# Kernel optimization log

Hardware: AMD Instinct MI355X
Metric: run time of the kernel (lower is better)

Reference implementation:

```python
import jax, jax.numpy as jnp
import numpy as np

B, N, DIM, H, D = 1, 1024, 512, 8, 64
BC, BS, K, W = 16, 16, 8, 256   # compress blk, selection blk, top-k blocks, sliding window
C = N // BC                     # number of compression / selection blocks
SCALE = D ** -0.5
EPS = 1e-6
NEG = -1e30


def rmsnorm(x):
    return x * jax.lax.rsqrt(jnp.mean(x * x, axis=-1, keepdims=True) + EPS)


def rope(x):  # x: [B,H,N,D], GPT-NeoX style half rotation
    half = D // 2
    inv = 1.0 / (10000.0 ** (jnp.arange(half, dtype=jnp.float32) / half))
    ang = jnp.arange(x.shape[2], dtype=jnp.float32)[:, None] * inv
    cos, sin = jnp.cos(ang), jnp.sin(ang)
    x1, x2 = x[..., :half], x[..., half:]
    return jnp.concatenate([x1 * cos - x2 * sin, x2 * cos + x1 * sin], axis=-1).astype(x.dtype)


def setup_inputs():
    key = jax.random.key(0)
    ks = jax.random.split(key, 24)
    w = lambda k, shape, fan: jax.random.normal(k, shape, jnp.float32) * (fan ** -0.5)
    return {
        'x':  jax.random.normal(ks[0], (B, N, DIM), jnp.float32),
        've': jax.random.normal(ks[1], (B, N, DIM), jnp.float32),
        'x0': jax.random.normal(ks[2], (B, N, DIM), jnp.float32),
        'lambdas': jnp.array([1.0, 0.0], jnp.float32),
        'Wq': w(ks[3], (DIM, H * D), DIM),
        'Wk': w(ks[4], (DIM, H * D), DIM),
        'Wv': w(ks[5], (DIM, H * D), DIM),
        'Wo': w(ks[6], (H * D, DIM), H * D),
        'Wg': w(ks[7], (DIM, 3 * H), DIM),
        'k_pos': w(ks[8], (H, BC, D), D),
        'v_pos': w(ks[9], (H, BC, D), D),
        'Wck': w(ks[10], (BC * D, D), BC * D),
        'bck': jnp.zeros((D,), jnp.float32),
        'Wcv': w(ks[11], (BC * D, D), BC * D),
        'bcv': jnp.zeros((D,), jnp.float32),
        'k_mem': w(ks[12], (H, 1, D), D),
        'v_mem': w(ks[13], (H, 1, D), D),
        'W1': w(ks[14], (DIM, 4 * DIM), DIM),
        'W2': w(ks[15], (4 * DIM, DIM), 4 * DIM),
    }


def _nsa_attn(xn, Wq, Wk, Wv, Wo, Wg, k_pos, v_pos, Wck, bck, Wcv, bcv, k_mem, v_mem):
    q = (xn @ Wq).reshape(B, N, H, D).transpose(0, 2, 1, 3)   # [B,H,N,D]
    k = (xn @ Wk).reshape(B, N, H, D).transpose(0, 2, 1, 3)
    v = (xn @ Wv).reshape(B, N, H, D).transpose(0, 2, 1, 3)
    q, k = rope(q), rope(k)
    i_idx = jnp.arange(N)

    # ---- compressed branch: pool kv into blocks via learned linear + intra-block pos emb ----
    kb = k.reshape(B, H, C, BC, D) + k_pos[None, :, None]
    vb = v.reshape(B, H, C, BC, D) + v_pos[None, :, None]
    ck = kb.reshape(B, H, C, BC * D) @ Wck + bck              # [B,H,C,D]
    cv = vb.reshape(B, H, C, BC * D) @ Wcv + bcv
    ckf = jnp.concatenate([jnp.broadcast_to(k_mem[None], (B, H, 1, D)), ck], axis=2)
    cvf = jnp.concatenate([jnp.broadcast_to(v_mem[None], (B, H, 1, D)), cv], axis=2)
    csim = jnp.einsum('bhid,bhjd->bhij', q, ckf) * SCALE      # [B,H,N,C+1]
    past = ((jnp.arange(C) + 1) * BC - 1)[None, :] < i_idx[:, None]   # block fully in the past
    cmask = jnp.concatenate([jnp.ones((N, 1), bool), past], axis=1)   # mem kv always visible
    cattn = jax.nn.softmax(jnp.where(cmask[None, None], csim, NEG), axis=-1)
    c_out = jnp.einsum('bhij,bhjd->bhid', cattn, cvf)

    # ---- fine selection branch: top-K blocks by compressed attention importance ----
    imp = jnp.where(past[None, None], cattn[..., 1:], NEG)    # [B,H,N,C]
    vals, sel = jax.lax.top_k(imp, K)                         # [B,H,N,K]
    valid = vals >= 0.0                                       # drop picks among masked blocks
    kb_f = k.reshape(B, H, C, BS, D)
    vb_f = v.reshape(B, H, C, BS, D)
    k_sel = jnp.take_along_axis(kb_f[:, :, None], sel[..., None, None], axis=3)  # [B,H,N,K,BS,D]
    v_sel = jnp.take_along_axis(vb_f[:, :, None], sel[..., None, None], axis=3)
    own = i_idx // BS                                         # query's own block, causal inside
    k_fine = jnp.concatenate([k_sel, kb_f[:, :, own][:, :, :, None]], axis=3)    # [B,H,N,K+1,BS,D]
    v_fine = jnp.concatenate([v_sel, vb_f[:, :, own][:, :, :, None]], axis=3)
    offs = jnp.arange(BS)
    m_sel = (sel[..., None] * BS + offs <= i_idx[None, None, :, None, None]) & valid[..., None]
    m_own = jnp.broadcast_to((own[:, None] * BS + offs <= i_idx[:, None])[None, None, :, None], (B, H, N, 1, BS))
    m_fine = jnp.concatenate([m_sel, m_own], axis=3)
    fsim = jnp.where(m_fine, jnp.einsum('bhnd,bhnksd->bhnks', q, k_fine) * SCALE, NEG)
    fattn = jax.nn.softmax(fsim.reshape(B, H, N, (K + 1) * BS), axis=-1).reshape(B, H, N, K + 1, BS)
    f_out = jnp.einsum('bhnks,bhnksd->bhnd', fattn, v_fine)

    # ---- sliding window branch ----
    smask = (i_idx[None, :] <= i_idx[:, None]) & (i_idx[:, None] - i_idx[None, :] < W)
    ssim = jnp.where(smask[None, None], jnp.einsum('bhid,bhjd->bhij', q, k) * SCALE, NEG)
    s_out = jnp.einsum('bhij,bhjd->bhid', jax.nn.softmax(ssim, axis=-1), v)

    # ---- per-head sigmoid gates combine the three strategies ----
    gates = jax.nn.sigmoid(xn @ Wg).reshape(B, N, H, 3).transpose(0, 2, 1, 3)  # [B,H,N,3]
    o = gates[..., 0:1] * c_out + gates[..., 1:2] * f_out + gates[..., 2:3] * s_out
    return o.transpose(0, 2, 1, 3).reshape(B, N, H * D) @ Wo


def reference(x, ve, x0, lambdas, Wq, Wk, Wv, Wo, Wg, k_pos, v_pos, Wck, bck, Wcv, bcv, k_mem, v_mem, W1, W2):
    # ve is accepted by NSABlock.forward but never consumed in this block
    x = lambdas[0] * x + lambdas[1] * x0
    x = x + _nsa_attn(rmsnorm(x), Wq, Wk, Wv, Wo, Wg, k_pos, v_pos, Wck, bck, Wcv, bcv, k_mem, v_mem)
    x = x + jnp.square(jax.nn.relu(rmsnorm(x) @ W1)) @ W2
    return x
```

## Files before the change

kernel.cpp:

```cpp
#include <hip/hip_runtime.h>
#include <math.h>

#define NTOK 1024
#define DIMM 512
#define NH 8
#define HD 64
#define BCB 16
#define BSB 16
#define KSEL 8
#define WWIN 256
#define CBLK 64
#define SCALE 0.125f
#define EPSV 1e-6f
#define NEGV -1e30f

typedef short bf16x8 __attribute__((ext_vector_type(8)));
typedef float f32x4 __attribute__((ext_vector_type(4)));

__device__ inline ushort f2b(float f) {
  union { float f; unsigned int u; } c; c.f = f;
  unsigned int u = c.u;
  return (ushort)((u + 0x7FFFu + ((u >> 16) & 1u)) >> 16);
}
__device__ inline float b2f(ushort h) {
  union { unsigned int u; float f; } c; c.u = ((unsigned int)h) << 16;
  return c.f;
}

__device__ inline float wred_max(float v) {
#pragma unroll
  for (int off = 1; off < 64; off <<= 1) v = fmaxf(v, __shfl_xor(v, off));
  return v;
}
__device__ inline float wred_sum(float v) {
#pragma unroll
  for (int off = 1; off < 64; off <<= 1) v += __shfl_xor(v, off);
  return v;
}

__global__ void __launch_bounds__(256)
k_resid_rms(const float* __restrict__ x, const float* __restrict__ x0,
            const float* __restrict__ lam, float* __restrict__ xr,
            float* __restrict__ xn) {
  int row = blockIdx.x, tid = threadIdx.x;
  float l0 = lam[0], l1 = lam[1];
  size_t b = (size_t)row * DIMM;
  float a0 = l0 * x[b + tid]       + l1 * x0[b + tid];
  float a1 = l0 * x[b + tid + 256] + l1 * x0[b + tid + 256];
  xr[b + tid] = a0; xr[b + tid + 256] = a1;
  float ss = a0 * a0 + a1 * a1;
  __shared__ float sm[8];
  for (int o = 32; o > 0; o >>= 1) ss += __shfl_down(ss, o);
  int lane = tid & 63, wid = tid >> 6;
  if (lane == 0) sm[wid] = ss;
  __syncthreads();
  if (tid == 0) {
    float s = sm[0] + sm[1] + sm[2] + sm[3];
    sm[0] = rsqrtf(s / (float)DIMM + EPSV);
  }
  __syncthreads();
  float r = sm[0];
  xn[b + tid] = a0 * r; xn[b + tid + 256] = a1 * r;
}

__global__ void __launch_bounds__(256)
k_rms_bf(const float* __restrict__ xin, ushort* __restrict__ y) {
  int row = blockIdx.x, tid = threadIdx.x;
  size_t b = (size_t)row * DIMM;
  float a0 = xin[b + tid], a1 = xin[b + tid + 256];
  float ss = a0 * a0 + a1 * a1;
  __shared__ float sm[8];
  for (int o = 32; o > 0; o >>= 1) ss += __shfl_down(ss, o);
  int lane = tid & 63, wid = tid >> 6;
  if (lane == 0) sm[wid] = ss;
  __syncthreads();
  if (tid == 0) {
    float s = sm[0] + sm[1] + sm[2] + sm[3];
    sm[0] = rsqrtf(s / (float)DIMM + EPSV);
  }
  __syncthreads();
  float r = sm[0];
  y[b + tid] = f2b(a0 * r); y[b + tid + 256] = f2b(a1 * r);
}

struct WtrDesc { const float* src; ushort* dh; ushort* dl; int K; int Nsrc; int Npad; };
struct WtrPack { WtrDesc d[9]; int cum[9]; };

__global__ void __launch_bounds__(256)
k_wtr_all(WtrPack pk) {
  int gb = blockIdx.x;
  int e = 0;
  while (gb >= pk.cum[e]) e++;
  int start = e ? pk.cum[e - 1] : 0;
  WtrDesc dd = pk.d[e];
  int local = gb - start;
  int XT = dd.Npad >> 5;
  int bx = local % XT, by = local / XT;
  __shared__ float t[32][33];
  int n0 = bx * 32, k0 = by * 32;
  int tx = threadIdx.x, ty = threadIdx.y;
#pragma unroll
  for (int i = 0; i < 32; i += 8)
    t[ty + i][tx] = (n0 + tx < dd.Nsrc)
        ? dd.src[(size_t)(k0 + ty + i) * dd.Nsrc + n0 + tx] : 0.f;
  __syncthreads();
#pragma unroll
  for (int i = 0; i < 32; i += 8) {
    float vv = t[tx][ty + i];
    ushort h = f2b(vv);
    size_t di = (size_t)(n0 + ty + i) * dd.K + k0 + tx;
    dd.dh[di] = h;
    if (dd.dl) dd.dl[di] = f2b(vv - b2f(h));
  }
}

__global__ void __launch_bounds__(256)
k_gemm_w1(const ushort* __restrict__ A, const ushort* __restrict__ BT,
          ushort* __restrict__ Co) {
  const int Kd = 512, Nd = 2048;
  __shared__ ushort As[128 * 40];
  __shared__ ushort Bs[64 * 40];
  int tid = threadIdx.x;
  int lane = tid & 63, w = tid >> 6;
  int rb = blockIdx.y * 128, cb = blockIdx.x * 64;
  int wm = (w >> 1) * 64, wn = (w & 1) * 32;
  int quad = lane >> 4, l15 = lane & 15;
  int srA = tid >> 1, scA = (tid & 1) * 16;
  int srB = tid >> 2, scB = (tid & 3) * 8;

  f32x4 acc[4][2];
#pragma unroll
  for (int i = 0; i < 4; i++)
#pragma unroll
    for (int j = 0; j < 2; j++) acc[i][j] = (f32x4){0.f, 0.f, 0.f, 0.f};

  const ushort* ap = A  + (size_t)(rb + srA) * Kd + scA;
  const ushort* bp = BT + (size_t)(cb + srB) * Kd + scB;
  ushort* aw = &As[srA * 40 + scA];
  ushort* bw = &Bs[srB * 40 + scB];

  int4 pa0 = *(const int4*)ap;
  int4 pa1 = *(const int4*)(ap + 8);
  int4 pb  = *(const int4*)bp;

  for (int k0 = 0; k0 < Kd; k0 += 32) {
    if (k0) __syncthreads();
    *(int4*)aw = pa0; *(int4*)(aw + 8) = pa1;
    *(int4*)bw = pb;
    __syncthreads();
    if (k0 + 32 < Kd) {
      pa0 = *(const int4*)(ap + k0 + 32);
      pa1 = *(const int4*)(ap + k0 + 40);
      pb  = *(const int4*)(bp + k0 + 32);
    }
    bf16x8 af[4], bfr[2];
#pragma unroll
    for (int t = 0; t < 4; t++)
      af[t] = *(const bf16x8*)&As[(wm + t * 16 + l15) * 40 + quad * 8];
#pragma unroll
    for (int t = 0; t < 2; t++)
      bfr[t] = *(const bf16x8*)&Bs[(wn + t * 16 + l15) * 40 + quad * 8];
#pragma unroll
    for (int i = 0; i < 4; i++)
#pragma unroll
      for (int j = 0; j < 2; j++)
        acc[i][j] = __builtin_amdgcn_mfma_f32_16x16x32_bf16(af[i], bfr[j],
                                                            acc[i][j], 0, 0, 0);
  }

#pragma unroll
  for (int i = 0; i < 4; i++) {
#pragma unroll
    for (int j = 0; j < 2; j++) {
      int col = cb + wn + j * 16 + l15;
#pragma unroll
      for (int r = 0; r < 4; r++) {
        int row = rb + wm + i * 16 + quad * 4 + r;
        float t = fmaxf(acc[i][j][r], 0.f);
        Co[(size_t)row * Nd + col] = f2b(t * t);
      }
    }
  }
}

__global__ void __launch_bounds__(256)
k_gemm_w2(const ushort* __restrict__ A, const ushort* __restrict__ BT,
          float* __restrict__ P0, float* __restrict__ P1) {
  const int Kd = 2048;
  __shared__ ushort As[64 * 40];
  __shared__ ushort Bs[64 * 40];
  int tid = threadIdx.x;
  int lane = tid & 63, w = tid >> 6;
  int rb = blockIdx.y * 64, cb = blockIdx.x * 64;
  int kb = blockIdx.z * 1024;
  int wm = (w >> 1) * 32, wn = (w & 1) * 32;
  int quad = lane >> 4, l15 = lane & 15;
  int srow = tid >> 2, scol = (tid & 3) * 8;

  f32x4 acc[2][2];
#pragma unroll
  for (int i = 0; i < 2; i++)
#pragma unroll
    for (int j = 0; j < 2; j++) acc[i][j] = (f32x4){0.f, 0.f, 0.f, 0.f};

  const ushort* ap = A  + (size_t)(rb + srow) * Kd + kb + scol;
  const ushort* bp = BT + (size_t)(cb + srow) * Kd + kb + scol;
  ushort* aw = &As[srow * 40 + scol];
  ushort* bw = &Bs[srow * 40 + scol];

  int4 pa = *(const int4*)ap;
  int4 pb = *(const int4*)bp;

  for (int k0 = 0; k0 < 1024; k0 += 32) {
    if (k0) __syncthreads();
    *(int4*)aw = pa;
    *(int4*)bw = pb;
    __syncthreads();
    if (k0 + 32 < 1024) {
      pa = *(const int4*)(ap + k0 + 32);
      pb = *(const int4*)(bp + k0 + 32);
    }
    bf16x8 af[2], bfr[2];
#pragma unroll
    for (int t = 0; t < 2; t++) {
      af[t]  = *(const bf16x8*)&As[(wm + t * 16 + l15) * 40 + quad * 8];
      bfr[t] = *(const bf16x8*)&Bs[(wn + t * 16 + l15) * 40 + quad * 8];
    }
#pragma unroll
    for (int i = 0; i < 2; i++)
#pragma unroll
      for (int j = 0; j < 2; j++)
        acc[i][j] = __builtin_amdgcn_mfma_f32_16x16x32_bf16(af[i], bfr[j],
                                                            acc[i][j], 0, 0, 0);
  }

  float* pbuf = blockIdx.z ? P1 : P0;
#pragma unroll
  for (int i = 0; i < 2; i++) {
#pragma unroll
    for (int j = 0; j < 2; j++) {
      int col = cb + wn + j * 16 + l15;
#pragma unroll
      for (int r = 0; r < 4; r++) {
        int row = rb + wm + i * 16 + quad * 4 + r;
        pbuf[(size_t)row * 512 + col] = acc[i][j][r];
      }
    }
  }
}

__global__ void __launch_bounds__(256)
k_w2fin(const float* __restrict__ x2, const float* __restrict__ p0,
        const float* __restrict__ p1, float* __restrict__ out) {
  int idx = blockIdx.x * 256 + threadIdx.x;
  out[idx] = x2[idx] + p0[idx] + p1[idx];
}

__global__ void __launch_bounds__(256)
k_gemm_wo(const float* __restrict__ cg, const float* __restrict__ fg,
          const float* __restrict__ sg, const float* __restrict__ gates,
          const ushort* __restrict__ BT, const float* __restrict__ Res,
          float* __restrict__ Co) {
  __shared__ ushort As[64 * 40];
  __shared__ ushort Bs[64 * 40];
  int tid = threadIdx.x;
  int lane = tid & 63, wave = tid >> 6;
  int rb = blockIdx.y * 64, cb = blockIdx.x * 64;
  int wm = (wave >> 1) * 32, wn = (wave & 1) * 32;
  int q = lane >> 4, l15 = lane & 15;
  int srow = tid >> 2, scol = (tid & 3) * 8;

  f32x4 acc[2][2];
#pragma unroll
  for (int i = 0; i < 2; i++)
#pragma unroll
    for (int j = 0; j < 2; j++) acc[i][j] = (f32x4){0.f, 0.f, 0.f, 0.f};

  int row = rb + srow;
  const ushort* bp = BT + (size_t)(cb + srow) * 512 + scol;
  ushort* aw = &As[srow * 40 + scol];
  ushort* bw = &Bs[srow * 40 + scol];

  for (int k0 = 0; k0 < 512; k0 += 32) {
    int colb = k0 + scol;
    int hh = colb >> 6;
    const float* gp = gates + (size_t)row * 24 + hh * 3;
    float g0 = gp[0], g1 = gp[1], g2 = gp[2];
    size_t off = (size_t)row * 512 + colb;
    float4 c0 = *(const float4*)(cg + off), c1 = *(const float4*)(cg + off + 4);
    float4 f0 = *(const float4*)(fg + off), f1 = *(const float4*)(fg + off + 4);
    float4 s0 = *(const float4*)(sg + off), s1 = *(const float4*)(sg + off + 4);
    float va[8] = {g0 * c0.x + g1 * f0.x + g2 * s0.x,
                   g0 * c0.y + g1 * f0.y + g2 * s0.y,
                   g0 * c0.z + g1 * f0.z + g2 * s0.z,
                   g0 * c0.w + g1 * f0.w + g2 * s0.w,
                   g0 * c1.x + g1 * f1.x + g2 * s1.x,
                   g0 * c1.y + g1 * f1.y + g2 * s1.y,
                   g0 * c1.z + g1 * f1.z + g2 * s1.z,
                   g0 * c1.w + g1 * f1.w + g2 * s1.w};
    ushort h[8];
#pragma unroll
    for (int e = 0; e < 8; e++) h[e] = f2b(va[e]);
    *(int4*)aw = *(int4*)h;
    *(int4*)bw = *(const int4*)(bp + k0);
    __syncthreads();
    bf16x8 af[2], bfr[2];
#pragma unroll
    for (int t = 0; t < 2; t++) {
      af[t]  = *(const bf16x8*)&As[(wm + t * 16 + l15) * 40 + q * 8];
      bfr[t] = *(const bf16x8*)&Bs[(wn + t * 16 + l15) * 40 + q * 8];
    }
#pragma unroll
    for (int i = 0; i < 2; i++)
#pragma unroll
      for (int j = 0; j < 2; j++)
        acc[i][j] = __builtin_amdgcn_mfma_f32_16x16x32_bf16(af[i], bfr[j],
                                                            acc[i][j], 0, 0, 0);
    __syncthreads();
  }

#pragma unroll
  for (int i = 0; i < 2; i++) {
#pragma unroll
    for (int j = 0; j < 2; j++) {
      int col = cb + wn + j * 16 + l15;
#pragma unroll
      for (int r = 0; r < 4; r++) {
        int rr = rb + wm + i * 16 + q * 4 + r;
        Co[(size_t)rr * 512 + col] = acc[i][j][r] + Res[(size_t)rr * 512 + col];
      }
    }
  }
}

__global__ void __launch_bounds__(256)
k_gemm_qkv(const float* __restrict__ A, const ushort* __restrict__ BTh,
           const ushort* __restrict__ BTl, float* __restrict__ Co,
           float* __restrict__ vhm, float* __restrict__ gates, int Kd) {
  __shared__ ushort Ash[64 * 40];
  __shared__ ushort Asl[64 * 40];
  __shared__ ushort Bsh[64 * 40];
  __shared__ ushort Bsl[64 * 40];
  int tid = threadIdx.x;
  int lane = tid & 63, wave = tid >> 6;
  int rb = blockIdx.y * 64, cb = blockIdx.x * 64;
  int wm = (wave >> 1) * 32, wn = (wave & 1) * 32;
  int q = lane >> 4, l15 = lane & 15;
  int srow = tid >> 2, scol = (tid & 3) * 8;

  f32x4 acc[2][2];
#pragma unroll
  for (int i = 0; i < 2; i++)
#pragma unroll
    for (int j = 0; j < 2; j++) acc[i][j] = (f32x4){0.f, 0.f, 0.f, 0.f};

  const float*  ap  = A   + (size_t)(rb + srow) * Kd + scol;
  const ushort* bph = BTh + (size_t)(cb + srow) * Kd + scol;
  const ushort* bpl = BTl + (size_t)(cb + srow) * Kd + scol;
  ushort* awh = &Ash[srow * 40 + scol];
  ushort* awl = &Asl[srow * 40 + scol];
  ushort* bwh = &Bsh[srow * 40 + scol];
  ushort* bwl = &Bsl[srow * 40 + scol];

  for (int k0 = 0; k0 < Kd; k0 += 32) {
    float4 a0 = *(const float4*)(ap + k0);
    float4 a1 = *(const float4*)(ap + k0 + 4);
    float va[8] = {a0.x, a0.y, a0.z, a0.w, a1.x, a1.y, a1.z, a1.w};
    ushort hh[8], hl[8];
#pragma unroll
    for (int e = 0; e < 8; e++) {
      hh[e] = f2b(va[e]);
      hl[e] = f2b(va[e] - b2f(hh[e]));
    }
    *(int4*)awh = *(int4*)hh;
    *(int4*)awl = *(int4*)hl;
    *(int4*)bwh = *(const int4*)(bph + k0);
    *(int4*)bwl = *(const int4*)(bpl + k0);
    __syncthreads();
    bf16x8 afh[2], afl[2], bfh[2], bfl[2];
#pragma unroll
    for (int t = 0; t < 2; t++) {
      int ar = (wm + t * 16 + l15) * 40 + q * 8;
      int br = (wn + t * 16 + l15) * 40 + q * 8;
      afh[t] = *(const bf16x8*)&Ash[ar];
      afl[t] = *(const bf16x8*)&Asl[ar];
      bfh[t] = *(const bf16x8*)&Bsh[br];
      bfl[t] = *(const bf16x8*)&Bsl[br];
    }
#pragma unroll
    for (int i = 0; i < 2; i++)
#pragma unroll
      for (int j = 0; j < 2; j++) {
        acc[i][j] = __builtin_amdgcn_mfma_f32_16x16x32_bf16(afh[i], bfh[j],
                                                            acc[i][j], 0, 0, 0);
        acc[i][j] = __builtin_amdgcn_mfma_f32_16x16x32_bf16(afh[i], bfl[j],
                                                            acc[i][j], 0, 0, 0);
        acc[i][j] = __builtin_amdgcn_mfma_f32_16x16x32_bf16(afl[i], bfh[j],
                                                            acc[i][j], 0, 0, 0);
      }
    __syncthreads();
  }

  const size_t NW = (size_t)NTOK * DIMM;
#pragma unroll
  for (int i = 0; i < 2; i++) {
#pragma unroll
    for (int j = 0; j < 2; j++) {
      int col = cb + wn + j * 16 + l15;
#pragma unroll
      for (int r = 0; r < 4; r++) {
        int row = rb + wm + i * 16 + q * 4 + r;
        float vv = acc[i][j][r];
        if (cb >= 1536) {
          int c24 = col - 1536;
          if (c24 < 24)
            gates[(size_t)row * 24 + c24] = 1.f / (1.f + expf(-vv));
        } else if (col >= 1024) {
          int c = col - 1024;
          vhm[(size_t)(c >> 6) * 65536 + (size_t)row * 64 + (c & 63)] = vv;
        } else {
          Co[(size_t)(col >> 9) * NW + (size_t)row * 512 + (col & 511)] = vv;
        }
      }
    }
  }
}

__global__ void __launch_bounds__(256)
k_rope(float* __restrict__ q, const float* __restrict__ k,
       float* __restrict__ khm, ushort* __restrict__ khm_bf,
       const float* __restrict__ vhm, ushort* __restrict__ vhm_bf) {
  int idx = blockIdx.x * 256 + threadIdx.x;
  int seg = idx >> 18;
  if (seg >= 2) {
    int ci = idx - 524288;
    if (ci < 131072) {
      float4 t = *(const float4*)(vhm + (size_t)ci * 4);
      ushort4 u = {f2b(t.x), f2b(t.y), f2b(t.z), f2b(t.w)};
      *(ushort4*)(vhm_bf + (size_t)ci * 4) = u;
    }
    return;
  }
  int r = idx & 262143;
  int j = r & 31;
  int h = (r >> 5) & 7;
  int n = r >> 8;
  float inv = powf(10000.f, -(float)j / 32.f);
  float ang = (float)n * inv;
  float sn, cs;
  sincosf(ang, &sn, &cs);
  size_t base = (size_t)n * DIMM + h * HD + j;
  if (seg == 0) {
    float x1 = q[base], x2 = q[base + 32];
    q[base] = x1 * cs - x2 * sn;
    q[base + 32] = x2 * cs + x1 * sn;
  } else {
    float x1 = k[base], x2 = k[base + 32];
    float o1 = x1 * cs - x2 * sn;
    float o2 = x2 * cs + x1 * sn;
    size_t ob = (size_t)h * 65536 + (size_t)n * 64 + j;
    khm[ob] = o1;
    khm[ob + 32] = o2;
    khm_bf[ob] = f2b(o1);
    khm_bf[ob + 32] = f2b(o2);
  }
}

__global__ void __launch_bounds__(256)
k_ckcv_m(const float* __restrict__ khm, const float* __restrict__ vhm,
         const float* __restrict__ k_pos, const float* __restrict__ v_pos,
         const ushort* __restrict__ WckTh, const ushort* __restrict__ WckTl,
         const ushort* __restrict__ WcvTh, const ushort* __restrict__ WcvTl,
         const float* __restrict__ bck, const float* __restrict__ bcv,
         float* __restrict__ ckb, float* __restrict__ cvb) {
  int h = blockIdx.x, kv = blockIdx.y;
  const float* src = kv ? vhm : khm;
  const float* pos = kv ? v_pos : k_pos;
  const ushort* WTh = kv ? WcvTh : WckTh;
  const ushort* WTl = kv ? WcvTl : WckTl;
  const float* bias = kv ? bcv : bck;
  float* outp = kv ? cvb : ckb;

  __shared__ ushort Ash[64 * 72], Asl[64 * 72];
  __shared__ ushort Bsh[64 * 72], Bsl[64 * 72];
  int tid = threadIdx.x;
  int lane = tid & 63, wave = tid >> 6;
  int wm = (wave >> 1) * 32, wn = (wave & 1) * 32;
  int q = lane >> 4, l15 = lane & 15;
  int srow = tid >> 2;
  int e0 = (tid & 3) * 16;

  f32x4 acc[2][2];
#pragma unroll
  for (int i = 0; i < 2; i++)
#pragma unroll
    for (int j = 0; j < 2; j++) acc[i][j] = (f32x4){0.f, 0.f, 0.f, 0.f};

  for (int t = 0; t < 16; t++) {
    const float* ar = src + (size_t)h * 65536 + (size_t)(srow * 16 + t) * 64 + e0;
    const float* pr = pos + (size_t)(h * 16 + t) * HD + e0;
    ushort hh[16], hl[16];
#pragma unroll
    for (int u = 0; u < 4; u++) {
      float4 av = *(const float4*)(ar + u * 4);
      float4 pv = *(const float4*)(pr + u * 4);
      float vals[4] = {av.x + pv.x, av.y + pv.y, av.z + pv.z, av.w + pv.w};
#pragma unroll
      for (int e = 0; e < 4; e++) {
        ushort hb = f2b(vals[e]);
        hh[u * 4 + e] = hb;
        hl[u * 4 + e] = f2b(vals[e] - b2f(hb));
      }
    }
    *(int4*)&Ash[srow * 72 + e0]     = *(int4*)&hh[0];
    *(int4*)&Ash[srow * 72 + e0 + 8] = *(int4*)&hh[8];
    *(int4*)&Asl[srow * 72 + e0]     = *(int4*)&hl[0];
    *(int4*)&Asl[srow * 72 + e0 + 8] = *(int4*)&hl[8];
    const ushort* bh = WTh + (size_t)srow * 1024 + t * 64 + e0;
    const ushort* bl = WTl + (size_t)srow * 1024 + t * 64 + e0;
    *(int4*)&Bsh[srow * 72 + e0]     = *(const int4*)bh;
    *(int4*)&Bsh[srow * 72 + e0 + 8] = *(const int4*)(bh + 8);
    *(int4*)&Bsl[srow * 72 + e0]     = *(const int4*)bl;
    *(int4*)&Bsl[srow * 72 + e0 + 8] = *(const int4*)(bl + 8);
    __syncthreads();
#pragma unroll
    for (int sub = 0; sub < 2; sub++) {
      bf16x8 afh[2], afl[2], bfh[2], bfl[2];
#pragma unroll
      for (int ti = 0; ti < 2; ti++) {
        int ar2 = (wm + ti * 16 + l15) * 72 + sub * 32 + q * 8;
        int br2 = (wn + ti * 16 + l15) * 72 + sub * 32 + q * 8;
        afh[ti] = *(const bf16x8*)&Ash[ar2];
        afl[ti] = *(const bf16x8*)&Asl[ar2];
        bfh[ti] = *(const bf16x8*)&Bsh[br2];
        bfl[ti] = *(const bf16x8*)&Bsl[br2];
      }
#pragma unroll
      for (int i = 0; i < 2; i++)
#pragma unroll
        for (int j = 0; j < 2; j++) {
          acc[i][j] = __builtin_amdgcn_mfma_f32_16x16x32_bf16(afh[i], bfh[j],
                                                              acc[i][j], 0, 0, 0);
          acc[i][j] = __builtin_amdgcn_mfma_f32_16x16x32_bf16(afh[i], bfl[j],
                                                              acc[i][j], 0, 0, 0);
          acc[i][j] = __builtin_amdgcn_mfma_f32_16x16x32_bf16(afl[i], bfh[j],
                                                              acc[i][j], 0, 0, 0);
        }
    }
    __syncthreads();
  }

#pragma unroll
  for (int i = 0; i < 2; i++) {
#pragma unroll
    for (int j = 0; j < 2; j++) {
      int d = wn + j * 16 + l15;
      float bv = bias[d];
#pragma unroll
      for (int r = 0; r < 4; r++) {
        int c = wm + i * 16 + q * 4 + r;
        outp[((size_t)h * 64 + c) * 64 + d] = acc[i][j][r] + bv;
      }
    }
  }
}

__global__ void __launch_bounds__(256)
k_cmp(const float* __restrict__ qg, const float* __restrict__ ckb,
      const float* __restrict__ cvb, const float* __restrict__ k_mem,
      const float* __restrict__ v_mem, float* __restrict__ cout,
      int* __restrict__ sel) {
  int h = blockIdx.y, i0 = blockIdx.x * 16;
  int tid = threadIdx.x, lane = tid & 63, w = tid >> 6;
  __shared__ float ckt[64][65];
  __shared__ float cvs[64][65];
  __shared__ float qs[16][64];
  __shared__ float kms[64], vms[64];
  __shared__ float sp[4][64];

#pragma unroll
  for (int r = 0; r < 4; r++) {
    int f = r * 256 + tid;
    int c = f >> 4, d0 = (f & 15) * 4;
    float4 t = *(const float4*)(ckb + ((size_t)h * 64 + c) * 64 + d0);
    ckt[d0][c] = t.x; ckt[d0 + 1][c] = t.y; ckt[d0 + 2][c] = t.z; ckt[d0 + 3][c] = t.w;
    float4 u = *(const float4*)(cvb + ((size_t)h * 64 + c) * 64 + d0);
    cvs[c][d0] = u.x; cvs[c][d0 + 1] = u.y; cvs[c][d0 + 2] = u.z; cvs[c][d0 + 3] = u.w;
  }
  {
    int r = tid >> 4, d0 = (tid & 15) * 4;
    float4 t = *(const float4*)(qg + (size_t)(i0 + r) * DIMM + h * HD + d0);
    qs[r][d0] = t.x; qs[r][d0 + 1] = t.y; qs[r][d0 + 2] = t.z; qs[r][d0 + 3] = t.w;
  }
  if (tid < 64) kms[tid] = k_mem[h * HD + tid];
  else if (tid < 128) vms[tid - 64] = v_mem[h * HD + tid - 64];
  __syncthreads();

  for (int s = 0; s < 4; s++) {
    int ql = w * 4 + s, qi = i0 + ql;
    float dot = 0.f, dm = 0.f;
#pragma unroll 8
    for (int e = 0; e < 64; e++) {
      float qe = qs[ql][e];
      dot = fmaf(qe, ckt[e][lane], dot);
      dm  = fmaf(qe, kms[e], dm);
    }
    bool vis = (lane * BCB + BCB - 1) < qi;
    float sj = vis ? dot * SCALE : NEGV;
    float smem = dm * SCALE;
    float m = wred_max(fmaxf(sj, smem));
    float p = expf(sj - m);
    float pmem = expf(smem - m);
    float l = wred_sum(p) + pmem;
    float inv = 1.f / l;

    float impv = vis ? p : NEGV;
#pragma unroll
    for (int kk = 0; kk < KSEL; kk++) {
      float bv = impv; int bi = lane;
#pragma unroll
      for (int off = 32; off > 0; off >>= 1) {
        float ov = __shfl_xor(bv, off);
        int   oi = __shfl_xor(bi, off);
        if (ov > bv || (ov == bv && oi < bi)) { bv = ov; bi = oi; }
      }
      if (lane == 0) sel[((size_t)h * NTOK + qi) * KSEL + kk] = (bv >= 0.f) ? bi : -1;
      if (lane == bi) impv = NEGV;
    }

    sp[w][lane] = p;
    float od = pmem * vms[lane];
#pragma unroll 8
    for (int j = 0; j < 64; j++) od = fmaf(sp[w][j], cvs[j][lane], od);
    cout[(size_t)qi * DIMM + h * HD + lane] = od * inv;
  }
}

__global__ void __launch_bounds__(256)
k_swin(const float* __restrict__ qg, const ushort* __restrict__ khm_bf,
       const ushort* __restrict__ vhm_bf, float* __restrict__ sout) {
  int h = blockIdx.y, i0 = blockIdx.x * 64;
  int tid = threadIdx.x, lane = tid & 63, w = tid >> 6;
  int quad = lane >> 4, l15 = lane & 15;

  __shared__ ushort Kt[64 * 72];
  __shared__ ushort VT[64 * 72];
  __shared__ ushort Qs[64 * 72];
  __shared__ ushort Ps[4][16 * 72];

#pragma unroll
  for (int it = 0; it < 4; it++) {
    int f = it * 256 + tid;
    int r = f >> 4, d0 = (f & 15) * 4;
    float4 t = *(const float4*)(qg + (size_t)(i0 + r) * DIMM + h * HD + d0);
    ushort4 u = {f2b(t.x), f2b(t.y), f2b(t.z), f2b(t.w)};
    *(ushort4*)&Qs[r * 72 + d0] = u;
  }

  int lo = i0 - (WWIN - 1); if (lo < 0) lo = 0;
  int jb_lo = lo >> 6, jb_hi = (i0 + 63) >> 6;

  float mrow[4], lrow[4];
  f32x4 Of[4];
#pragma unroll
  for (int r = 0; r < 4; r++) { mrow[r] = NEGV; lrow[r] = 0.f; }
#pragma unroll
  for (int d = 0; d < 4; d++) Of[d] = (f32x4){0.f, 0.f, 0.f, 0.f};

  for (int jb = jb_lo; jb <= jb_hi; jb++) {
    __syncthreads();
#pragma unroll
    for (int it = 0; it < 2; it++) {
      int f = it * 256 + tid;
      int r = f >> 3, c8 = (f & 7) * 8;
      const ushort* kp = khm_bf + (size_t)h * 65536 + (size_t)(jb * 64 + r) * 64 + c8;
      *(int4*)&Kt[r * 72 + c8] = *(const int4*)kp;
      const ushort* vp = vhm_bf + (size_t)h * 65536 + (size_t)(jb * 64 + r) * 64 + c8;
      ushort vv[8];
      *(int4*)vv = *(const int4*)vp;
#pragma unroll
      for (int e = 0; e < 8; e++) VT[(c8 + e) * 72 + r] = vv[e];
    }
    __syncthreads();

    bf16x8 qa[2];
#pragma unroll
    for (int c = 0; c < 2; c++)
      qa[c] = *(const bf16x8*)&Qs[(w * 16 + l15) * 72 + c * 32 + quad * 8];

    f32x4 sc[4];
#pragma unroll
    for (int ks = 0; ks < 4; ks++) {
      f32x4 a = (f32x4){0.f, 0.f, 0.f, 0.f};
#pragma unroll
      for (int c = 0; c < 2; c++) {
        bf16x8 kb = *(const bf16x8*)&Kt[(ks * 16 + l15) * 72 + c * 32 + quad * 8];
        a = __builtin_amdgcn_mfma_f32_16x16x32_bf16(qa[c], kb, a, 0, 0, 0);
      }
      sc[ks] = a;
    }

    float pm[4][4], rmax[4];
#pragma unroll
    for (int r = 0; r < 4; r++) rmax[r] = NEGV;
#pragma unroll
    for (int ks = 0; ks < 4; ks++) {
      int gj = jb * 64 + ks * 16 + l15;
#pragma unroll
      for (int r = 0; r < 4; r++) {
        int qi = i0 + w * 16 + quad * 4 + r;
        bool vis = (gj <= qi) && (qi - gj < WWIN);
        float s = vis ? sc[ks][r] * SCALE : NEGV;
        pm[ks][r] = s;
        rmax[r] = fmaxf(rmax[r], s);
      }
    }
#pragma unroll
    for (int off = 1; off < 16; off <<= 1)
#pragma unroll
      for (int r = 0; r < 4; r++)
        rmax[r] = fmaxf(rmax[r], __shfl_xor(rmax[r], off));

    float alpha[4], rsum[4];
#pragma unroll
    for (int r = 0; r < 4; r++) {
      float newm = fmaxf(mrow[r], rmax[r]);
      alpha[r] = expf(mrow[r] - newm);
      mrow[r] = newm;
      rsum[r] = 0.f;
    }
#pragma unroll
    for (int ks = 0; ks < 4; ks++)
#pragma unroll
      for (int r = 0; r < 4; r++) {
        float p = expf(pm[ks][r] - mrow[r]);
        pm[ks][r] = p;
        rsum[r] += p;
      }
#pragma unroll
    for (int off = 1; off < 16; off <<= 1)
#pragma unroll
      for (int r = 0; r < 4; r++)
        rsum[r] += __shfl_xor(rsum[r], off);
#pragma unroll
    for (int r = 0; r < 4; r++)
      lrow[r] = lrow[r] * alpha[r] + rsum[r];

#pragma unroll
    for (int ks = 0; ks < 4; ks++)
#pragma unroll
      for (int r = 0; r < 4; r++)
        Ps[w][(quad * 4 + r) * 72 + ks * 16 + l15] = f2b(pm[ks][r]);
#pragma unroll
    for (int d = 0; d < 4; d++)
#pragma unroll
      for (int r = 0; r < 4; r++)
        Of[d][r] *= alpha[r];

#pragma unroll
    for (int c = 0; c < 2; c++) {
      bf16x8 pa = *(const bf16x8*)&Ps[w][l15 * 72 + c * 32 + quad * 8];
#pragma unroll
      for (int d = 0; d < 4; d++) {
        bf16x8 vb = *(const bf16x8*)&VT[(d * 16 + l15) * 72 + c * 32 + quad * 8];
        Of[d] = __builtin_amdgcn_mfma_f32_16x16x32_bf16(pa, vb, Of[d], 0, 0, 0);
      }
    }
  }

#pragma unroll
  for (int d = 0; d < 4; d++)
#pragma unroll
    for (int r = 0; r < 4; r++) {
      int qi = i0 + w * 16 + quad * 4 + r;
      sout[(size_t)qi * DIMM + h * HD + d * 16 + l15] = Of[d][r] / lrow[r];
    }
}

__global__ void __launch_bounds__(256)
k_fine(const float* __restrict__ qg, const ushort* __restrict__ khm_bf,
       const ushort* __restrict__ vhm_bf, const int* __restrict__ sel,
       float* __restrict__ fout) {
  int i = blockIdx.x, h = blockIdx.y;
  int tid = threadIdx.x, lane = tid & 63, w = tid >> 6;
  __shared__ float qsh[64];
  __shared__ ushort vsb[144 * 64];
  __shared__ float sp[144];
  __shared__ int selS[8];
  __shared__ float mred[4], sredS[4];
  __shared__ float pacc[4][64];

  int own = i >> 4;
  if (tid < 64) qsh[tid] = qg[(size_t)i * DIMM + h * HD + tid];
  if (tid >= 64 && tid < 72)
    selS[tid - 64] = sel[((size_t)h * NTOK + i) * KSEL + tid - 64];
  __syncthreads();

  const ushort* kbase = khm_bf + (size_t)h * 65536;
  const ushort* vbase = vhm_bf + (size_t)h * 65536;

#pragma unroll
  for (int it = 0; it < 5; it++) {
    int idx = it * 256 + tid;
    if (idx < 1152) {
      int row = idx >> 3, c8 = (idx & 7) * 8;
      int kk = row >> 4;
      int bidx = (kk < KSEL) ? selS[kk] : own;
      if (bidx < 0) bidx = 0;
      *(int4*)&vsb[row * 64 + c8] =
          *(const int4*)(vbase + (size_t)(bidx * BSB + (row & 15)) * 64 + c8);
    }
  }

  float s_loc = NEGV;
  bool active = (tid < 144);
  if (active) {
    int kk = tid >> 4;
    int bidx; bool vis;
    if (kk < KSEL) {
      bidx = selS[kk];
      vis = (bidx >= 0);
      if (!vis) bidx = 0;
    } else {
      bidx = own;
      vis = (tid - 128) <= (i & 15);
    }
    const ushort* kr = kbase + (size_t)(bidx * BSB + (tid & 15)) * 64;
    float dot = 0.f;
#pragma unroll
    for (int e8 = 0; e8 < 8; e8++) {
      ushort kv[8];
      *(int4*)kv = *(const int4*)(kr + e8 * 8);
#pragma unroll
      for (int e = 0; e < 8; e++)
        dot = fmaf(qsh[e8 * 8 + e], b2f(kv[e]), dot);
    }
    s_loc = vis ? dot * SCALE : NEGV;
  }
  float mw = wred_max(s_loc);
  if (lane == 0) mred[w] = mw;
  __syncthreads();
  float m = fmaxf(fmaxf(mred[0], mred[1]), fmaxf(mred[2], mred[3]));
  float p = active ? expf(s_loc - m) : 0.f;
  float sw = wred_sum(p);
  if (lane == 0) sredS[w] = sw;
  if (active) sp[tid] = p;
  __syncthreads();
  float l = sredS[0] + sredS[1] + sredS[2] + sredS[3];

  float acc = 0.f;
  int j0 = w * 36;
#pragma unroll 6
  for (int jj = 0; jj < 36; jj++) {
    int j = j0 + jj;
    acc = fmaf(sp[j], b2f(vsb[j * 64 + lane]), acc);
  }
  pacc[w][lane] = acc;
  __syncthreads();
  if (w == 0)
    fout[(size_t)i * DIMM + h * HD + lane] =
        (pacc[0][lane] + pacc[1][lane] + pacc[2][lane] + pacc[3][lane]) / l;
}

extern "C" void kernel_launch(void* const* d_in, const int* in_sizes, int n_in,
                              void* d_out, int out_size, void* d_ws, size_t ws_size,
                              hipStream_t stream) {
  const float* x     = (const float*)d_in[0];
  const float* ve    = (const float*)d_in[1]; (void)ve;
  const float* x0    = (const float*)d_in[2];
  const float* lam   = (const float*)d_in[3];
  const float* Wq    = (const float*)d_in[4];
  const float* Wk    = (const float*)d_in[5];
  const float* Wv    = (const float*)d_in[6];
  const float* Wo    = (const float*)d_in[7];
  const float* Wg    = (const float*)d_in[8];
  const float* k_pos = (const float*)d_in[9];
  const float* v_pos = (const float*)d_in[10];
  const float* Wck   = (const float*)d_in[11];
  const float* bck   = (const float*)d_in[12];
  const float* Wcv   = (const float*)d_in[13];
  const float* bcv   = (const float*)d_in[14];
  const float* k_mem = (const float*)d_in[15];
  const float* v_mem = (const float*)d_in[16];
  const float* W1    = (const float*)d_in[17];
  const float* W2    = (const float*)d_in[18];
  float* out = (float*)d_out;
  float* ws  = (float*)d_ws;

  const size_t NW = (size_t)NTOK * DIMM;
  float* xr    = ws;
  float* xn    = ws + 1 * NW;
  float* q     = ws + 2 * NW;
  float* k     = ws + 3 * NW;
  float* vhm   = ws + 4 * NW;
  float* coutb = ws + 5 * NW;
  float* foutb = ws + 6 * NW;
  float* soutb = ws + 7 * NW;
  float* x2    = ws + 8 * NW;
  float* khm   = x2;
  float* gates = ws + 9 * NW;
  float* ckb   = gates + 32768;
  float* cvb   = ckb + 32768;
  int*   selb  = (int*)(cvb + 32768);
  ushort* qkvTh = (ushort*)(cvb + 32768 + 65536);
  ushort* qkvTl = qkvTh + 1600 * 512;
  ushort* WoT   = qkvTl + 1600 * 512;
  ushort* W1T   = WoT   + 512 * 512;
  ushort* W2T   = W1T   + 2048 * 512;
  ushort* WckTh = W2T   + 512 * 2048;
  ushort* WckTl = WckTh + 64 * 1024;
  ushort* WcvTh = WckTl + 64 * 1024;
  ushort* WcvTl = WcvTh + 64 * 1024;
  ushort* ybf = (ushort*)xr;
  ushort* h1b = (ushort*)q;
  float* p0 = xn;
  float* p1 = vhm;
  ushort* khm_bf = (ushort*)xn;
  ushort* vhm_bf = khm_bf + 524288;

  WtrPack pk;
  pk.d[0] = {Wq, qkvTh,              qkvTl,              512, 512,  512};
  pk.d[1] = {Wk, qkvTh + 512 * 512,  qkvTl + 512 * 512,  512, 512,  512};
  pk.d[2] = {Wv, qkvTh + 1024 * 512, qkvTl + 1024 * 512, 512, 512,  512};
  pk.d[3] = {Wo, WoT, nullptr,  512, 512,  512};
  pk.d[4] = {W1, W1T, nullptr,  512, 2048, 2048};
  pk.d[5] = {W2, W2T, nullptr, 2048, 512,  512};
  pk.d[6] = {Wck, WckTh, WckTl, 1024, 64, 64};
  pk.d[7] = {Wcv, WcvTh, WcvTl, 1024, 64, 64};
  pk.d[8] = {Wg, qkvTh + 1536 * 512, qkvTl + 1536 * 512, 512, 24, 64};
  int cum = 0;
  for (int e = 0; e < 9; e++) {
    cum += (pk.d[e].Npad / 32) * (pk.d[e].K / 32);
    pk.cum[e] = cum;
  }
  k_wtr_all<<<cum, dim3(32, 8), 0, stream>>>(pk);

  k_resid_rms<<<NTOK, 256, 0, stream>>>(x, x0, lam, xr, xn);

  k_gemm_qkv<<<dim3(25, NTOK / 64), 256, 0, stream>>>(
      xn, qkvTh, qkvTl, q, vhm, gates, 512);
  k_rope<<<2560, 256, 0, stream>>>(q, k, khm, khm_bf, vhm, vhm_bf);

  k_ckcv_m<<<dim3(NH, 2), 256, 0, stream>>>(khm, vhm, k_pos, v_pos,
                                            WckTh, WckTl, WcvTh, WcvTl,
                                            bck, bcv, ckb, cvb);
  k_cmp<<<dim3(NTOK / 16, NH), 256, 0, stream>>>(q, ckb, cvb, k_mem, v_mem,
                                                 coutb, selb);
  k_swin<<<dim3(NTOK / 64, NH), 256, 0, stream>>>(q, khm_bf, vhm_bf, soutb);
  k_fine<<<dim3(NTOK, NH), 256, 0, stream>>>(q, khm_bf, vhm_bf, selb, foutb);

  k_gemm_wo<<<dim3(512 / 64, NTOK / 64), 256, 0, stream>>>(
      coutb, foutb, soutb, gates, WoT, xr, x2);

  k_rms_bf<<<NTOK, 256, 0, stream>>>(x2, ybf);
  k_gemm_w1<<<dim3(2048 / 64, NTOK / 128), 256, 0, stream>>>(ybf, W1T, h1b);
  k_gemm_w2<<<dim3(512 / 64, NTOK / 64, 2), 256, 0, stream>>>(h1b, W2T, p0, p1);
  k_w2fin<<<NW / 256, 256, 0, stream>>>(x2, p0, p1, out);
}
```

Before: 279.7 us.

## Split-K Wo GEMM, split ckcv and swin grids, drop split-bf16 for V/gates

The Wo projection is split over K into two partial buffers, and the residual add is fused into the following RMSNorm kernel. The compression-weight GEMM is split into two M-halves and the sliding-window kernel uses 32-row tiles with 128 threads, both to raise block counts on small grids. The QKV GEMM skips the hi/lo correction MFMAs for column blocks at or above 1024 (V and gates), which cuts compute but lowers precision for V.

Result: faster. 270.1 us (-3.4%).

```diff
diff --git a/kernel.cpp b/kernel.cpp
--- a/kernel.cpp
+++ b/kernel.cpp
@@ -64,10 +64,14 @@
 }
 
 __global__ void __launch_bounds__(256)
-k_rms_bf(const float* __restrict__ xin, ushort* __restrict__ y) {
+k_rms_bf(const float* __restrict__ xr, const float* __restrict__ p0,
+         const float* __restrict__ p1, float* __restrict__ x2,
+         ushort* __restrict__ y) {
   int row = blockIdx.x, tid = threadIdx.x;
   size_t b = (size_t)row * DIMM;
-  float a0 = xin[b + tid], a1 = xin[b + tid + 256];
+  float a0 = xr[b + tid]       + p0[b + tid]       + p1[b + tid];
+  float a1 = xr[b + tid + 256] + p0[b + tid + 256] + p1[b + tid + 256];
+  x2[b + tid] = a0; x2[b + tid + 256] = a1;
   float ss = a0 * a0 + a1 * a1;
   __shared__ float sm[8];
   for (int o = 32; o > 0; o >>= 1) ss += __shfl_down(ss, o);
@@ -259,13 +263,14 @@
 __global__ void __launch_bounds__(256)
 k_gemm_wo(const float* __restrict__ cg, const float* __restrict__ fg,
           const float* __restrict__ sg, const float* __restrict__ gates,
-          const ushort* __restrict__ BT, const float* __restrict__ Res,
-          float* __restrict__ Co) {
+          const ushort* __restrict__ BT, float* __restrict__ P0,
+          float* __restrict__ P1) {
   __shared__ ushort As[64 * 40];
   __shared__ ushort Bs[64 * 40];
   int tid = threadIdx.x;
   int lane = tid & 63, wave = tid >> 6;
   int rb = blockIdx.y * 64, cb = blockIdx.x * 64;
+  int kb = blockIdx.z * 256;
   int wm = (wave >> 1) * 32, wn = (wave & 1) * 32;
   int q = lane >> 4, l15 = lane & 15;
   int srow = tid >> 2, scol = (tid & 3) * 8;
@@ -277,12 +282,12 @@
     for (int j = 0; j < 2; j++) acc[i][j] = (f32x4){0.f, 0.f, 0.f, 0.f};
 
   int row = rb + srow;
-  const ushort* bp = BT + (size_t)(cb + srow) * 512 + scol;
+  const ushort* bp = BT + (size_t)(cb + srow) * 512 + kb + scol;
   ushort* aw = &As[srow * 40 + scol];
   ushort* bw = &Bs[srow * 40 + scol];
 
-  for (int k0 = 0; k0 < 512; k0 += 32) {
-    int colb = k0 + scol;
+  for (int k0 = 0; k0 < 256; k0 += 32) {
+    int colb = kb + k0 + scol;
     int hh = colb >> 6;
     const float* gp = gates + (size_t)row * 24 + hh * 3;
     float g0 = gp[0], g1 = gp[1], g2 = gp[2];
@@ -319,6 +324,7 @@
     __syncthreads();
   }
 
+  float* pbuf = blockIdx.z ? P1 : P0;
 #pragma unroll
   for (int i = 0; i < 2; i++) {
 #pragma unroll
@@ -327,7 +333,7 @@
 #pragma unroll
       for (int r = 0; r < 4; r++) {
         int rr = rb + wm + i * 16 + q * 4 + r;
-        Co[(size_t)rr * 512 + col] = acc[i][j][r] + Res[(size_t)rr * 512 + col];
+        pbuf[(size_t)rr * 512 + col] = acc[i][j][r];
       }
     }
   }
@@ -344,6 +350,7 @@
   int tid = threadIdx.x;
   int lane = tid & 63, wave = tid >> 6;
   int rb = blockIdx.y * 64, cb = blockIdx.x * 64;
+  const bool prec = (cb < 1024);
   int wm = (wave >> 1) * 32, wn = (wave & 1) * 32;
   int q = lane >> 4, l15 = lane & 15;
   int srow = tid >> 2, scol = (tid & 3) * 8;
@@ -368,14 +375,15 @@
     float va[8] = {a0.x, a0.y, a0.z, a0.w, a1.x, a1.y, a1.z, a1.w};
     ushort hh[8], hl[8];
 #pragma unroll
-    for (int e = 0; e < 8; e++) {
-      hh[e] = f2b(va[e]);
-      hl[e] = f2b(va[e] - b2f(hh[e]));
-    }
+    for (int e = 0; e < 8; e++) hh[e] = f2b(va[e]);
     *(int4*)awh = *(int4*)hh;
-    *(int4*)awl = *(int4*)hl;
     *(int4*)bwh = *(const int4*)(bph + k0);
-    *(int4*)bwl = *(const int4*)(bpl + k0);
+    if (prec) {
+#pragma unroll
+      for (int e = 0; e < 8; e++) hl[e] = f2b(va[e] - b2f(hh[e]));
+      *(int4*)awl = *(int4*)hl;
+      *(int4*)bwl = *(const int4*)(bpl + k0);
+    }
     __syncthreads();
     bf16x8 afh[2], afl[2], bfh[2], bfl[2];
 #pragma unroll
@@ -383,9 +391,11 @@
       int ar = (wm + t * 16 + l15) * 40 + q * 8;
       int br = (wn + t * 16 + l15) * 40 + q * 8;
       afh[t] = *(const bf16x8*)&Ash[ar];
-      afl[t] = *(const bf16x8*)&Asl[ar];
       bfh[t] = *(const bf16x8*)&Bsh[br];
-      bfl[t] = *(const bf16x8*)&Bsl[br];
+      if (prec) {
+        afl[t] = *(const bf16x8*)&Asl[ar];
+        bfl[t] = *(const bf16x8*)&Bsl[br];
+      }
     }
 #pragma unroll
     for (int i = 0; i < 2; i++)
@@ -393,10 +403,12 @@
       for (int j = 0; j < 2; j++) {
         acc[i][j] = __builtin_amdgcn_mfma_f32_16x16x32_bf16(afh[i], bfh[j],
                                                             acc[i][j], 0, 0, 0);
-        acc[i][j] = __builtin_amdgcn_mfma_f32_16x16x32_bf16(afh[i], bfl[j],
-                                                            acc[i][j], 0, 0, 0);
-        acc[i][j] = __builtin_amdgcn_mfma_f32_16x16x32_bf16(afl[i], bfh[j],
-                                                            acc[i][j], 0, 0, 0);
+        if (prec) {
+          acc[i][j] = __builtin_amdgcn_mfma_f32_16x16x32_bf16(afh[i], bfl[j],
+                                                              acc[i][j], 0, 0, 0);
+          acc[i][j] = __builtin_amdgcn_mfma_f32_16x16x32_bf16(afl[i], bfh[j],
+                                                              acc[i][j], 0, 0, 0);
+        }
       }
     __syncthreads();
   }
@@ -473,7 +485,7 @@
          const ushort* __restrict__ WcvTh, const ushort* __restrict__ WcvTl,
          const float* __restrict__ bck, const float* __restrict__ bcv,
          float* __restrict__ ckb, float* __restrict__ cvb) {
-  int h = blockIdx.x, kv = blockIdx.y;
+  int h = blockIdx.x, kv = blockIdx.y, mh = blockIdx.z;
   const float* src = kv ? vhm : khm;
   const float* pos = kv ? v_pos : k_pos;
   const ushort* WTh = kv ? WcvTh : WckTh;
@@ -481,27 +493,26 @@
   const float* bias = kv ? bcv : bck;
   float* outp = kv ? cvb : ckb;
 
-  __shared__ ushort Ash[64 * 72], Asl[64 * 72];
+  __shared__ ushort Ash[32 * 72], Asl[32 * 72];
   __shared__ ushort Bsh[64 * 72], Bsl[64 * 72];
   int tid = threadIdx.x;
   int lane = tid & 63, wave = tid >> 6;
-  int wm = (wave >> 1) * 32, wn = (wave & 1) * 32;
-  int q = lane >> 4, l15 = lane & 15;
-  int srow = tid >> 2;
-  int e0 = (tid & 3) * 16;
-
-  f32x4 acc[2][2];
-#pragma unroll
-  for (int i = 0; i < 2; i++)
-#pragma unroll
-    for (int j = 0; j < 2; j++) acc[i][j] = (f32x4){0.f, 0.f, 0.f, 0.f};
+  int wmi = wave >> 1, wnj = wave & 1;
+  int quad = lane >> 4, l15 = lane & 15;
+  int arow = tid >> 3, ae0 = (tid & 7) * 8;
+  int brow = tid >> 2, be0 = (tid & 3) * 16;
+
+  f32x4 acc[2];
+#pragma unroll
+  for (int j = 0; j < 2; j++) acc[j] = (f32x4){0.f, 0.f, 0.f, 0.f};
 
   for (int t = 0; t < 16; t++) {
-    const float* ar = src + (size_t)h * 65536 + (size_t)(srow * 16 + t) * 64 + e0;
-    const float* pr = pos + (size_t)(h * 16 + t) * HD + e0;
-    ushort hh[16], hl[16];
-#pragma unroll
-    for (int u = 0; u < 4; u++) {
+    const float* ar = src + (size_t)h * 65536 +
+                      (size_t)((mh * 32 + arow) * 16 + t) * 64 + ae0;
+    const float* pr = pos + (size_t)(h * 16 + t) * HD + ae0;
+    ushort hh[8], hl[8];
+#pragma unroll
+    for (int u = 0; u < 2; u++) {
       float4 av = *(const float4*)(ar + u * 4);
       float4 pv = *(const float4*)(pr + u * 4);
       float vals[4] = {av.x + pv.x, av.y + pv.y, av.z + pv.z, av.w + pv.w};
@@ -512,55 +523,41 @@
         hl[u * 4 + e] = f2b(vals[e] - b2f(hb));
       }
     }
-    *(int4*)&Ash[srow * 72 + e0]     = *(int4*)&hh[0];
-    *(int4*)&Ash[srow * 72 + e0 + 8] = *(int4*)&hh[8];
-    *(int4*)&Asl[srow * 72 + e0]     = *(int4*)&hl[0];
-    *(int4*)&Asl[srow * 72 + e0 + 8] = *(int4*)&hl[8];
-    const ushort* bh = WTh + (size_t)srow * 1024 + t * 64 + e0;
-    const ushort* bl = WTl + (size_t)srow * 1024 + t * 64 + e0;
-    *(int4*)&Bsh[srow * 72 + e0]     = *(const int4*)bh;
-    *(int4*)&Bsh[srow * 72 + e0 + 8] = *(const int4*)(bh + 8);
-    *(int4*)&Bsl[srow * 72 + e0]     = *(const int4*)bl;
-    *(int4*)&Bsl[srow * 72 + e0 + 8] = *(const int4*)(bl + 8);
+    *(int4*)&Ash[arow * 72 + ae0] = *(int4*)hh;
+    *(int4*)&Asl[arow * 72 + ae0] = *(int4*)hl;
+    const ushort* bh = WTh + (size_t)brow * 1024 + t * 64 + be0;
+    const ushort* bl = WTl + (size_t)brow * 1024 + t * 64 + be0;
+    *(int4*)&Bsh[brow * 72 + be0]     = *(const int4*)bh;
+    *(int4*)&Bsh[brow * 72 + be0 + 8] = *(const int4*)(bh + 8);
+    *(int4*)&Bsl[brow * 72 + be0]     = *(const int4*)bl;
+    *(int4*)&Bsl[brow * 72 + be0 + 8] = *(const int4*)(bl + 8);
     __syncthreads();
 #pragma unroll
     for (int sub = 0; sub < 2; sub++) {
-      bf16x8 afh[2], afl[2], bfh[2], bfl[2];
-#pragma unroll
-      for (int ti = 0; ti < 2; ti++) {
-        int ar2 = (wm + ti * 16 + l15) * 72 + sub * 32 + q * 8;
-        int br2 = (wn + ti * 16 + l15) * 72 + sub * 32 + q * 8;
-        afh[ti] = *(const bf16x8*)&Ash[ar2];
-        afl[ti] = *(const bf16x8*)&Asl[ar2];
-        bfh[ti] = *(const bf16x8*)&Bsh[br2];
-        bfl[ti] = *(const bf16x8*)&Bsl[br2];
-      }
-#pragma unroll
-      for (int i = 0; i < 2; i++)
-#pragma unroll
-        for (int j = 0; j < 2; j++) {
-          acc[i][j] = __builtin_amdgcn_mfma_f32_16x16x32_bf16(afh[i], bfh[j],
-                                                              acc[i][j], 0, 0, 0);
-          acc[i][j] = __builtin_amdgcn_mfma_f32_16x16x32_bf16(afh[i], bfl[j],
-                                                              acc[i][j], 0, 0, 0);
-          acc[i][j] = __builtin_amdgcn_mfma_f32_16x16x32_bf16(afl[i], bfh[j],
-                                                              acc[i][j], 0, 0, 0);
-        }
+      int ar2 = (wmi * 16 + l15) * 72 + sub * 32 + quad * 8;
+      bf16x8 afh = *(const bf16x8*)&Ash[ar2];
+      bf16x8 afl = *(const bf16x8*)&Asl[ar2];
+#pragma unroll
+      for (int j = 0; j < 2; j++) {
+        int br2 = (wnj * 32 + j * 16 + l15) * 72 + sub * 32 + quad * 8;
+        bf16x8 bfh = *(const bf16x8*)&Bsh[br2];
+        bf16x8 bfl = *(const bf16x8*)&Bsl[br2];
+        acc[j] = __builtin_amdgcn_mfma_f32_16x16x32_bf16(afh, bfh, acc[j], 0, 0, 0);
+        acc[j] = __builtin_amdgcn_mfma_f32_16x16x32_bf16(afh, bfl, acc[j], 0, 0, 0);
+        acc[j] = __builtin_amdgcn_mfma_f32_16x16x32_bf16(afl, bfh, acc[j], 0, 0, 0);
+      }
     }
     __syncthreads();
   }
 
 #pragma unroll
-  for (int i = 0; i < 2; i++) {
-#pragma unroll
-    for (int j = 0; j < 2; j++) {
-      int d = wn + j * 16 + l15;
-      float bv = bias[d];
-#pragma unroll
-      for (int r = 0; r < 4; r++) {
-        int c = wm + i * 16 + q * 4 + r;
-        outp[((size_t)h * 64 + c) * 64 + d] = acc[i][j][r] + bv;
-      }
+  for (int j = 0; j < 2; j++) {
+    int d = wnj * 32 + j * 16 + l15;
+    float bv = bias[d];
+#pragma unroll
+    for (int r = 0; r < 4; r++) {
+      int c = mh * 32 + wmi * 16 + quad * 4 + r;
+      outp[((size_t)h * 64 + c) * 64 + d] = acc[j][r] + bv;
     }
   }
 }
@@ -636,29 +633,32 @@
   }
 }
 
-__global__ void __launch_bounds__(256)
+__global__ void __launch_bounds__(128)
 k_swin(const float* __restrict__ qg, const ushort* __restrict__ khm_bf,
        const ushort* __restrict__ vhm_bf, float* __restrict__ sout) {
-  int h = blockIdx.y, i0 = blockIdx.x * 64;
+  int h = blockIdx.y, i0 = blockIdx.x * 32;
   int tid = threadIdx.x, lane = tid & 63, w = tid >> 6;
   int quad = lane >> 4, l15 = lane & 15;
 
   __shared__ ushort Kt[64 * 72];
   __shared__ ushort VT[64 * 72];
-  __shared__ ushort Qs[64 * 72];
-  __shared__ ushort Ps[4][16 * 72];
-
-#pragma unroll
-  for (int it = 0; it < 4; it++) {
-    int f = it * 256 + tid;
-    int r = f >> 4, d0 = (f & 15) * 4;
-    float4 t = *(const float4*)(qg + (size_t)(i0 + r) * DIMM + h * HD + d0);
-    ushort4 u = {f2b(t.x), f2b(t.y), f2b(t.z), f2b(t.w)};
-    *(ushort4*)&Qs[r * 72 + d0] = u;
+  __shared__ ushort Qs[32 * 72];
+  __shared__ ushort Ps[2][16 * 72];
+
+#pragma unroll
+  for (int it = 0; it < 2; it++) {
+    int f = it * 128 + tid;
+    int r = f >> 3, d0 = (f & 7) * 8;
+    const float* qp = qg + (size_t)(i0 + r) * DIMM + h * HD + d0;
+    float4 t0 = *(const float4*)qp;
+    float4 t1 = *(const float4*)(qp + 4);
+    ushort u[8] = {f2b(t0.x), f2b(t0.y), f2b(t0.z), f2b(t0.w),
+                   f2b(t1.x), f2b(t1.y), f2b(t1.z), f2b(t1.w)};
+    *(int4*)&Qs[r * 72 + d0] = *(int4*)u;
   }
 
   int lo = i0 - (WWIN - 1); if (lo < 0) lo = 0;
-  int jb_lo = lo >> 6, jb_hi = (i0 + 63) >> 6;
+  int jb_lo = lo >> 6, jb_hi = (i0 + 31) >> 6;
 
   float mrow[4], lrow[4];
   f32x4 Of[4];
@@ -670,8 +670,8 @@
   for (int jb = jb_lo; jb <= jb_hi; jb++) {
     __syncthreads();
 #pragma unroll
-    for (int it = 0; it < 2; it++) {
-      int f = it * 256 + tid;
+    for (int it = 0; it < 4; it++) {
+      int f = it * 128 + tid;
       int r = f >> 3, c8 = (f & 7) * 8;
       const ushort* kp = khm_bf + (size_t)h * 65536 + (size_t)(jb * 64 + r) * 64 + c8;
       *(int4*)&Kt[r * 72 + c8] = *(const int4*)kp;
@@ -911,7 +911,9 @@
   ushort* WckTl = WckTh + 64 * 1024;
   ushort* WcvTh = WckTl + 64 * 1024;
   ushort* WcvTl = WcvTh + 64 * 1024;
-  ushort* ybf = (ushort*)xr;
+  float* p0w = k;
+  float* p1w = q;
+  ushort* ybf = (ushort*)soutb;
   ushort* h1b = (ushort*)q;
   float* p0 = xn;
   float* p1 = vhm;
@@ -941,18 +943,18 @@
       xn, qkvTh, qkvTl, q, vhm, gates, 512);
   k_rope<<<2560, 256, 0, stream>>>(q, k, khm, khm_bf, vhm, vhm_bf);
 
-  k_ckcv_m<<<dim3(NH, 2), 256, 0, stream>>>(khm, vhm, k_pos, v_pos,
-                                            WckTh, WckTl, WcvTh, WcvTl,
-                                            bck, bcv, ckb, cvb);
+  k_ckcv_m<<<dim3(NH, 2, 2), 256, 0, stream>>>(khm, vhm, k_pos, v_pos,
+                                               WckTh, WckTl, WcvTh, WcvTl,
+                                               bck, bcv, ckb, cvb);
   k_cmp<<<dim3(NTOK / 16, NH), 256, 0, stream>>>(q, ckb, cvb, k_mem, v_mem,
                                                  coutb, selb);
-  k_swin<<<dim3(NTOK / 64, NH), 256, 0, stream>>>(q, khm_bf, vhm_bf, soutb);
+  k_swin<<<dim3(NTOK / 32, NH), 128, 0, stream>>>(q, khm_bf, vhm_bf, soutb);
   k_fine<<<dim3(NTOK, NH), 256, 0, stream>>>(q, khm_bf, vhm_bf, selb, foutb);
 
-  k_gemm_wo<<<dim3(512 / 64, NTOK / 64), 256, 0, stream>>>(
-      coutb, foutb, soutb, gates, WoT, xr, x2);
-
-  k_rms_bf<<<NTOK, 256, 0, stream>>>(x2, ybf);
+  k_gemm_wo<<<dim3(512 / 64, NTOK / 64, 2), 256, 0, stream>>>(
+      coutb, foutb, soutb, gates, WoT, p0w, p1w);
+  k_rms_bf<<<NTOK, 256, 0, stream>>>(xr, p0w, p1w, x2, ybf);
+
   k_gemm_w1<<<dim3(2048 / 64, NTOK / 128), 256, 0, stream>>>(ybf, W1T, h1b);
   k_gemm_w2<<<dim3(512 / 64, NTOK / 64, 2), 256, 0, stream>>>(h1b, W2T, p0, p1);
   k_w2fin<<<NW / 256, 256, 0, stream>>>(x2, p0, p1, out);
```
